# Kernel optimization log

Measured on AMD Instinct MI355X. Metric: run time of the kernel, lower is better.

Reference implementation:

```python
import jax, jax.numpy as jnp
import numpy as np

D_MODEL = 1024
N_HEADS = 16
D_K = 64

def setup_inputs() -> dict:
    key = jax.random.key(0)
    k0, k1, k2, k3, k4 = jax.random.split(key, 5)
    B, S = 4, 4096
    std = 0.02
    x = jax.random.normal(k0, (B, S, D_MODEL), dtype=jnp.float32)
    # nn.Linear weights are [out, in]; init normal(0, 0.02) as in _init_weights
    W_q = std * jax.random.normal(k1, (N_HEADS * D_K, D_MODEL), dtype=jnp.float32)
    W_k = std * jax.random.normal(k2, (N_HEADS * D_K, D_MODEL), dtype=jnp.float32)
    W_v = std * jax.random.normal(k3, (N_HEADS * D_K, D_MODEL), dtype=jnp.float32)
    W_o = std * jax.random.normal(k4, (D_MODEL, N_HEADS * D_K), dtype=jnp.float32)
    return {"x": x, "W_q": W_q, "W_k": W_k, "W_v": W_v, "W_o": W_o}

def reference(x, W_q, W_k, W_v, W_o):
    B, S, _ = x.shape
    H, Dk = N_HEADS, D_K
    # projections (nn.Linear: x @ W.T), reshape to [B, S, H, Dk]
    q = (x @ W_q.T).reshape(B, S, H, Dk)
    k = (x @ W_k.T).reshape(B, S, H, Dk)
    v = (x @ W_v.T).reshape(B, S, H, Dk)
    scale = 1.0 / jnp.sqrt(jnp.float32(Dk))
    # No softmax between the two matmuls -> reassociate (QK^T)V = Q(K^TV),
    # identical math, O(S*d^2) instead of O(S^2*d).
    kv = jnp.einsum('bshd,bshe->bhde', k, v)          # [B, H, Dk, Dk]
    attn = jnp.einsum('bshd,bhde->bshe', q, kv) * scale  # [B, S, H, Dk]
    out = attn.reshape(B, S, H * Dk) @ W_o.T
    return out
```

## Files before the change

### kernel.cpp

```cpp
#include <hip/hip_runtime.h>
#include <hip/hip_bf16.h>
#include <cstdint>


typedef __bf16 bf16x8 __attribute__((ext_vector_type(8)));
typedef float f32x4 __attribute__((ext_vector_type(4)));
typedef unsigned short ushort_t;

__device__ inline void gld_lds16(const void* g, void* l) {
    __builtin_amdgcn_global_load_lds(
        (const __attribute__((address_space(1))) unsigned int*)g,
        (__attribute__((address_space(3))) unsigned int*)l,
        16, 0, 0);
}

__device__ inline ushort_t f2bf(float f) {
    uint32_t u = __float_as_uint(f);
    uint32_t r = (u + 0x7fffu + ((u >> 16) & 1u)) >> 16;
    return (ushort_t)r;
}
__device__ inline float bf2f(ushort_t u) {
    return __uint_as_float((uint32_t)u << 16);
}

__global__ __launch_bounds__(256)
void prep(const float* __restrict__ x, const float* __restrict__ Wk,
          const float* __restrict__ Wv, const float* __restrict__ Wq,
          ushort_t* __restrict__ xb, ushort_t* __restrict__ xbT,
          ushort_t* __restrict__ wkv, ushort_t* __restrict__ wqT)
{
    __shared__ ushort_t lt[64 * 66];
    const int id = blockIdx.x;
    const int t  = threadIdx.x;

    if (id < 4096) {
        const int s0 = (id & 255) * 64;
        const int i0 = (id >> 8) * 64;
#pragma unroll
        for (int c = 0; c < 4; ++c) {
            const int idx = c * 256 + t;
            const int r = idx >> 4, c4 = (idx & 15) * 4;
            const float4 f = *(const float4*)&x[(size_t)(s0 + r) * 1024 + i0 + c4];
            ushort4 o;
            o.x = f2bf(f.x); o.y = f2bf(f.y); o.z = f2bf(f.z); o.w = f2bf(f.w);
            *(ushort4*)&xb[(size_t)(s0 + r) * 1024 + i0 + c4] = o;
            *(uint32_t*)&lt[r * 66 + c4]     = (uint32_t)o.x | ((uint32_t)o.y << 16);
            *(uint32_t*)&lt[r * 66 + c4 + 2] = (uint32_t)o.z | ((uint32_t)o.w << 16);
        }
        __syncthreads();
#pragma unroll
        for (int c = 0; c < 4; ++c) {
            const int idx = c * 256 + t;
            const int ri = idx >> 4, s4 = (idx & 15) * 4;
            ushort4 o;
            o.x = lt[(s4 + 0) * 66 + ri];
            o.y = lt[(s4 + 1) * 66 + ri];
            o.z = lt[(s4 + 2) * 66 + ri];
            o.w = lt[(s4 + 3) * 66 + ri];
            *(ushort4*)&xbT[(size_t)(i0 + ri) * 16384 + s0 + s4] = o;
        }
        return;
    }

    if (id < 5120) {
        const int q  = id - 4096;
        const int qq = (q < 512) ? q : q - 512;
        const float* src = (q < 512) ? Wk : Wv;
        const float* s = src + (size_t)qq * 2048 + t * 8;
        ushort_t* d = wkv + (size_t)q * 2048 + t * 8;
        const float4 f0 = *(const float4*)(s);
        const float4 f1 = *(const float4*)(s + 4);
        ushort4 o0, o1;
        o0.x = f2bf(f0.x); o0.y = f2bf(f0.y); o0.z = f2bf(f0.z); o0.w = f2bf(f0.w);
        o1.x = f2bf(f1.x); o1.y = f2bf(f1.y); o1.z = f2bf(f1.z); o1.w = f2bf(f1.w);
        *(ushort4*)(d)     = o0;
        *(ushort4*)(d + 4) = o1;
        return;
    }

    const int id2 = id - 5120;
    const int r0 = (id2 >> 4) * 64;
    const int c0 = (id2 & 15) * 64;
#pragma unroll
    for (int c = 0; c < 4; ++c) {
        const int idx = c * 256 + t;
        const int r = idx >> 4, c4 = (idx & 15) * 4;
        const float4 f = *(const float4*)&Wq[(size_t)(r0 + r) * 1024 + c0 + c4];
        ushort4 o;
        o.x = f2bf(f.x); o.y = f2bf(f.y); o.z = f2bf(f.z); o.w = f2bf(f.w);
        *(uint32_t*)&lt[r * 66 + c4]     = (uint32_t)o.x | ((uint32_t)o.y << 16);
        *(uint32_t*)&lt[r * 66 + c4 + 2] = (uint32_t)o.z | ((uint32_t)o.w << 16);
    }
    __syncthreads();
#pragma unroll
    for (int c = 0; c < 4; ++c) {
        const int idx = c * 256 + t;
        const int ri = idx >> 4, s4 = (idx & 15) * 4;
        ushort4 o;
        o.x = lt[(s4 + 0) * 66 + ri];
        o.y = lt[(s4 + 1) * 66 + ri];
        o.z = lt[(s4 + 2) * 66 + ri];
        o.w = lt[(s4 + 3) * 66 + ri];
        *(ushort4*)&wqT[(size_t)(c0 + ri) * 1024 + r0 + s4] = o;
    }
}

template <typename OutT>
__global__ __launch_bounds__(256, 4)
void gemm_bt_n64(const ushort_t* __restrict__ A, int lda, long strideA,
                 const ushort_t* __restrict__ B, int ldb, long strideB,
                 OutT* __restrict__ C0, int ldc0, long strideC0, int K)
{
    __shared__ ushort_t lA[128 * 32];
    __shared__ ushort_t lB[64 * 32];

    const int t    = threadIdx.x;
    const int lane = t & 63;
    const int wid  = t >> 6;
    const int z    = blockIdx.z;

    A += (size_t)z * strideA;
    B += (size_t)z * strideB;

    const int m0 = blockIdx.x * 128;
    const int n0 = blockIdx.y * 64;

    const int wm = (wid >> 1) * 64;
    const int wn = (wid & 1) * 32;
    const int mr = lane & 15;
    const int q4 = lane >> 4;

    const int row_a = t >> 2;
    const int seg   = ((t & 3) ^ ((t >> 3) & 3)) * 8;
    const int csw   = (q4 ^ ((mr >> 1) & 3)) * 16;

    f32x4 acc[4][2] = {};

    for (int k0 = 0; k0 < K; k0 += 32) {
        __syncthreads();
        gld_lds16(A + (size_t)(m0 + row_a) * lda + k0 + seg,      (char*)lA + wid * 1024);
        gld_lds16(A + (size_t)(m0 + 64 + row_a) * lda + k0 + seg, (char*)lA + 4096 + wid * 1024);
        gld_lds16(B + (size_t)(n0 + row_a) * ldb + k0 + seg,      (char*)lB + wid * 1024);
        __syncthreads();

        bf16x8 af[4], bf[2];
#pragma unroll
        for (int i = 0; i < 4; ++i)
            af[i] = *(const bf16x8*)((const char*)lA + (wm + i * 16 + mr) * 64 + csw);
#pragma unroll
        for (int j = 0; j < 2; ++j)
            bf[j] = *(const bf16x8*)((const char*)lB + (wn + j * 16 + mr) * 64 + csw);
#pragma unroll
        for (int i = 0; i < 4; ++i)
#pragma unroll
            for (int j = 0; j < 2; ++j)
                acc[i][j] = __builtin_amdgcn_mfma_f32_16x16x32_bf16(af[i], bf[j], acc[i][j], 0, 0, 0);
    }

    OutT* Cw = C0 + (size_t)z * strideC0;
#pragma unroll
    for (int i = 0; i < 4; ++i) {
        const int rbase = m0 + wm + i * 16 + q4 * 4;
#pragma unroll
        for (int j = 0; j < 2; ++j) {
            const int col = n0 + wn + j * 16 + mr;
#pragma unroll
            for (int r = 0; r < 4; ++r) {
                const float v = acc[i][j][r];
                const size_t off = (size_t)(rbase + r) * ldc0 + col;
                if constexpr (sizeof(OutT) == 2) Cw[off] = f2bf(v);
                else                             Cw[off] = v;
            }
        }
    }
}

__global__ __launch_bounds__(256, 2)
void gemm_fin(const ushort_t* __restrict__ A, int lda, long strideA,
              const ushort_t* __restrict__ B, int ldb, long strideB,
              float* __restrict__ C, int ldc, long strideC, int K)
{
    __shared__ char lds[73728];

    const int t    = threadIdx.x;
    const int lane = t & 63;
    const int wid  = t >> 6;

    const int L  = blockIdx.x + (blockIdx.y << 4) + (blockIdx.z << 7);
    const int w  = ((L & 7) << 6) + (L >> 3);
    const int bx = w & 15, by = (w >> 4) & 7, z = w >> 7;

    A += (size_t)z * strideA;
    B += (size_t)z * strideB;

    const int m0 = bx * 256;
    const int n0 = by * 128;

    const int wr = wid >> 1;
    const int wn = wid & 1;
    const int mr = lane & 15;
    const int q4 = lane >> 4;

    const int NT = K >> 5;

    const int row_a = t >> 2;
    const int seg   = ((t & 3) ^ ((t >> 3) & 3)) * 8;
    const int csw   = (q4 ^ ((mr >> 1) & 3)) * 16;

    auto stage = [&](int tgt, int bsel) {
        if (tgt >= NT) return;
        char* base = lds + bsel * 24576 + wid * 1024;
        const ushort_t* gA = A + (size_t)(m0 + row_a) * lda + tgt * 32 + seg;
        gld_lds16(gA,                          base);
        gld_lds16(gA + ((size_t)lda << 6),     base + 4096);
        gld_lds16(gA + ((size_t)lda << 7),     base + 8192);
        gld_lds16(gA + (size_t)lda * 192,      base + 12288);
        const ushort_t* gB = B + (size_t)(n0 + row_a) * ldb + tgt * 32 + seg;
        gld_lds16(gB,                          base + 16384);
        gld_lds16(gB + ((size_t)ldb << 6),     base + 20480);
    };

    bf16x8 af[8], bf[4];
    f32x4 acc[8][4] = {};

    stage(0, 0);
    stage(1, 1);
    asm volatile("s_waitcnt vmcnt(6)" ::: "memory");
    __builtin_amdgcn_s_barrier();

    int cur = 0;
    for (int kt = 0; kt < NT; ++kt) {
        const char* buf = lds + cur * 24576;
#pragma unroll
        for (int i = 0; i < 8; ++i)
            af[i] = *(const bf16x8*)(buf + (wr * 128 + i * 16 + mr) * 64 + csw);
#pragma unroll
        for (int j = 0; j < 4; ++j)
            bf[j] = *(const bf16x8*)(buf + 16384 + (wn * 64 + j * 16 + mr) * 64 + csw);

        int b2 = cur + 2; if (b2 >= 3) b2 -= 3;
        stage(kt + 2, b2);

        asm volatile("s_waitcnt lgkmcnt(0)" ::: "memory");
        __builtin_amdgcn_sched_barrier(0);
        __builtin_amdgcn_s_setprio(1);
#pragma unroll
        for (int i = 0; i < 8; ++i)
#pragma unroll
            for (int j = 0; j < 4; ++j)
                acc[i][j] = __builtin_amdgcn_mfma_f32_16x16x32_bf16(
                    af[i], bf[j], acc[i][j], 0, 0, 0);
        __builtin_amdgcn_s_setprio(0);
        __builtin_amdgcn_sched_barrier(0);

        if (kt + 2 < NT)       asm volatile("s_waitcnt vmcnt(6)" ::: "memory");
        else if (kt + 2 == NT) asm volatile("s_waitcnt vmcnt(0)" ::: "memory");
        __builtin_amdgcn_s_barrier();
        if (++cur == 3) cur = 0;
    }

    float* Cw = C + (size_t)z * strideC;
#pragma unroll
    for (int i = 0; i < 8; ++i) {
        const int rbase = m0 + wr * 128 + i * 16 + q4 * 4;
#pragma unroll
        for (int j = 0; j < 4; ++j) {
            const int col = n0 + wn * 64 + j * 16 + mr;
#pragma unroll
            for (int r = 0; r < 4; ++r)
                Cw[(size_t)(rbase + r) * ldc + col] = acc[i][j][r];
        }
    }
}

__global__ __launch_bounds__(256, 2)
void gemm_gram(const ushort_t* __restrict__ X, ushort_t* __restrict__ Gp)
{
    __shared__ ushort_t lA[128 * 32];
    __shared__ ushort_t lB[128 * 32];

    const int t    = threadIdx.x;
    const int lane = t & 63;
    const int wid  = t >> 6;

    const int z  = blockIdx.x;
    const int bb = z >> 2, ks = z & 3;

    int ti = 0, rem = blockIdx.y;
    while (rem >= 8 - ti) { rem -= 8 - ti; ++ti; }
    const int tj = ti + rem;
    const int m0 = ti * 128;
    const int n0 = tj * 128;

    const ushort_t* A = X + (size_t)bb * 4096 + (size_t)ks * 1024;

    const int wm = (wid >> 1) * 64;
    const int wn = (wid & 1) * 64;
    const int mr = lane & 15;
    const int q4 = lane >> 4;

    const int row_a = t >> 2;
    const int seg   = ((t & 3) ^ ((t >> 3) & 3)) * 8;
    const int csw   = (q4 ^ ((mr >> 1) & 3)) * 16;

    f32x4 acc[4][4] = {};

    for (int k0 = 0; k0 < 1024; k0 += 32) {
        __syncthreads();
        gld_lds16(A + (size_t)(m0 + row_a) * 16384 + k0 + seg,      (char*)lA + wid * 1024);
        gld_lds16(A + (size_t)(m0 + 64 + row_a) * 16384 + k0 + seg, (char*)lA + 4096 + wid * 1024);
        gld_lds16(A + (size_t)(n0 + row_a) * 16384 + k0 + seg,      (char*)lB + wid * 1024);
        gld_lds16(A + (size_t)(n0 + 64 + row_a) * 16384 + k0 + seg, (char*)lB + 4096 + wid * 1024);
        __syncthreads();

        bf16x8 af[4], bf[4];
#pragma unroll
        for (int i = 0; i < 4; ++i)
            af[i] = *(const bf16x8*)((const char*)lA + (wm + i * 16 + mr) * 64 + csw);
#pragma unroll
        for (int j = 0; j < 4; ++j)
            bf[j] = *(const bf16x8*)((const char*)lB + (wn + j * 16 + mr) * 64 + csw);
#pragma unroll
        for (int i = 0; i < 4; ++i)
#pragma unroll
            for (int j = 0; j < 4; ++j)
                acc[i][j] = __builtin_amdgcn_mfma_f32_16x16x32_bf16(af[i], bf[j], acc[i][j], 0, 0, 0);
    }

    ushort_t* Cw = Gp + ((size_t)z << 20);
#pragma unroll
    for (int i = 0; i < 4; ++i) {
        const int rbase = m0 + wm + i * 16 + q4 * 4;
#pragma unroll
        for (int j = 0; j < 4; ++j) {
            const int col = n0 + wn + j * 16 + mr;
#pragma unroll
            for (int r = 0; r < 4; ++r)
                Cw[(size_t)(rbase + r) * 1024 + col] = f2bf(acc[i][j][r]);
        }
    }
}

__global__ __launch_bounds__(256)
void reduce_g_t(const ushort_t* __restrict__ Gp, ushort_t* __restrict__ G)
{
    __shared__ float acc[64 * 65];

    const int t  = threadIdx.x;
    const int b  = blockIdx.y;
    const int tr = blockIdx.x >> 4, tc = blockIdx.x & 15;
    const int sr = (tr <= tc) ? tr : tc;
    const int sc = (tr <= tc) ? tc : tr;
    const bool flip = tr > tc;

#pragma unroll
    for (int p = 0; p < 4; ++p) {
        const int idx = p * 256 + t;
        const int r = idx >> 4, c = (idx & 15) * 4;
        float a0 = 0.f, a1 = 0.f, a2 = 0.f, a3 = 0.f;
#pragma unroll
        for (int ksl = 0; ksl < 4; ++ksl) {
            const ushort4 u = *(const ushort4*)&Gp[((size_t)(b * 4 + ksl) << 20)
                                                   + (size_t)(sr * 64 + r) * 1024 + sc * 64 + c];
            a0 += bf2f(u.x); a1 += bf2f(u.y); a2 += bf2f(u.z); a3 += bf2f(u.w);
        }
        acc[r * 65 + c + 0] = a0;
        acc[r * 65 + c + 1] = a1;
        acc[r * 65 + c + 2] = a2;
        acc[r * 65 + c + 3] = a3;
    }
    __syncthreads();

#pragma unroll
    for (int p = 0; p < 4; ++p) {
        const int idx = p * 256 + t;
        const int r = idx >> 4, c = (idx & 15) * 4;
        float v0, v1, v2, v3;
        if (flip) {
            v0 = acc[(c + 0) * 65 + r];
            v1 = acc[(c + 1) * 65 + r];
            v2 = acc[(c + 2) * 65 + r];
            v3 = acc[(c + 3) * 65 + r];
        } else {
            v0 = acc[r * 65 + c + 0];
            v1 = acc[r * 65 + c + 1];
            v2 = acc[r * 65 + c + 2];
            v3 = acc[r * 65 + c + 3];
        }
        ushort4 o;
        o.x = f2bf(v0); o.y = f2bf(v1); o.z = f2bf(v2); o.w = f2bf(v3);
        *(ushort4*)&G[((size_t)b << 20) + (size_t)(tr * 64 + r) * 1024 + tc * 64 + c] = o;
    }
}

__global__ __launch_bounds__(256)
void kvblk(const ushort_t* __restrict__ H, const ushort_t* __restrict__ Wv,
           float* __restrict__ KVp)
{
    __shared__ ushort_t sH[64 * 132];
    __shared__ ushort_t sV[64 * 132];

    const int t  = threadIdx.x;
    const int is = blockIdx.x;
    const int bh = blockIdx.y;
    const int b  = bh >> 4, h = bh & 15;

    const ushort_t* Hp = H + ((size_t)b << 20) + (size_t)(h * 64) * 1024 + is * 128;
    const ushort_t* Vp = Wv + (size_t)(h * 64) * 1024 + is * 128;

#pragma unroll
    for (int i2 = 0; i2 < 8; ++i2) {
        const int ci = i2 * 256 + t;
        const int r = ci >> 5, c = (ci & 31) * 4;
        *(uint2*)&sH[r * 132 + c] = *(const uint2*)&Hp[(size_t)r * 1024 + c];
        *(uint2*)&sV[r * 132 + c] = *(const uint2*)&Vp[(size_t)r * 1024 + c];
    }
    __syncthreads();

    const int d0 = (t >> 4) * 4;
    const int e0 = (t & 15) * 4;
    float acc[4][4] = {};

#pragma unroll 2
    for (int i4 = 0; i4 < 128; i4 += 4) {
        uint2 hu[4], vu[4];
#pragma unroll
        for (int j = 0; j < 4; ++j) {
            hu[j] = *(const uint2*)&sH[(d0 + j) * 132 + i4];
            vu[j] = *(const uint2*)&sV[(e0 + j) * 132 + i4];
        }
        float hf[4][4], vf[4][4];
#pragma unroll
        for (int j = 0; j < 4; ++j) {
            hf[j][0] = __uint_as_float(hu[j].x << 16);
            hf[j][1] = __uint_as_float(hu[j].x & 0xffff0000u);
            hf[j][2] = __uint_as_float(hu[j].y << 16);
            hf[j][3] = __uint_as_float(hu[j].y & 0xffff0000u);
            vf[j][0] = __uint_as_float(vu[j].x << 16);
            vf[j][1] = __uint_as_float(vu[j].x & 0xffff0000u);
            vf[j][2] = __uint_as_float(vu[j].y << 16);
            vf[j][3] = __uint_as_float(vu[j].y & 0xffff0000u);
        }
#pragma unroll
        for (int ii = 0; ii < 4; ++ii)
#pragma unroll
            for (int di = 0; di < 4; ++di)
#pragma unroll
                for (int ej = 0; ej < 4; ++ej)
                    acc[di][ej] += hf[di][ii] * vf[ej][ii];
    }

    float* outp = KVp + ((size_t)(is * 64 + bh)) * 4096;
#pragma unroll
    for (int i = 0; i < 4; ++i) {
        float4 o; o.x = acc[i][0]; o.y = acc[i][1]; o.z = acc[i][2]; o.w = acc[i][3];
        *(float4*)&outp[(d0 + i) * 64 + e0] = o;
    }
}

__global__ __launch_bounds__(256)
void make_E8(const float* __restrict__ KVp, const float* __restrict__ Wo,
             ushort_t* __restrict__ Et)
{
    __shared__ float skv[64 * 65];
    __shared__ float swo[64 * 65];

    const int t  = threadIdx.x;
    const int bh = blockIdx.y;
    const int b  = bh >> 4, h = bh & 15;
    const int j0 = blockIdx.x * 64;

#pragma unroll
    for (int i = 0; i < 4; ++i) {
        const int idx = t + i * 256;
        const int r = idx >> 4, c = (idx & 15) * 4;
        float4 f; f.x = 0.f; f.y = 0.f; f.z = 0.f; f.w = 0.f;
#pragma unroll
        for (int is = 0; is < 8; ++is) {
            const float4 p = *(const float4*)&KVp[((size_t)(is * 64 + bh)) * 4096
                                                  + r * 64 + c];
            f.x += p.x; f.y += p.y; f.z += p.z; f.w += p.w;
        }
        skv[r * 65 + c + 0] = f.x;
        skv[r * 65 + c + 1] = f.y;
        skv[r * 65 + c + 2] = f.z;
        skv[r * 65 + c + 3] = f.w;
        const float4 g = *(const float4*)&Wo[(size_t)(j0 + r) * 1024 + h * 64 + c];
        swo[r * 65 + c + 0] = g.x;
        swo[r * 65 + c + 1] = g.y;
        swo[r * 65 + c + 2] = g.z;
        swo[r * 65 + c + 3] = g.w;
    }
    __syncthreads();

    const int d0 = (t & 15) * 4;
#pragma unroll
    for (int pass = 0; pass < 4; ++pass) {
        const int jloc = (t >> 4) + pass * 16;
        float s0 = 0.f, s1 = 0.f, s2 = 0.f, s3 = 0.f;
        const float* wrow = &swo[jloc * 65];
#pragma unroll 8
        for (int e = 0; e < 64; ++e) {
            const float w = wrow[e];
            s0 += skv[(d0 + 0) * 65 + e] * w;
            s1 += skv[(d0 + 1) * 65 + e] * w;
            s2 += skv[(d0 + 2) * 65 + e] * w;
            s3 += skv[(d0 + 3) * 65 + e] * w;
        }
        ushort4 o;
        o.x = f2bf(s0 * 0.125f);
        o.y = f2bf(s1 * 0.125f);
        o.z = f2bf(s2 * 0.125f);
        o.w = f2bf(s3 * 0.125f);
        *(ushort4*)&Et[((size_t)b * 1024 + j0 + jloc) * 1024 + h * 64 + d0] = o;
    }
}


extern "C" void kernel_launch(void* const* d_in, const int* in_sizes, int n_in,
                              void* d_out, int out_size, void* d_ws, size_t ws_size,
                              hipStream_t stream)
{
    const float* x  = (const float*)d_in[0];
    const float* Wq = (const float*)d_in[1];
    const float* Wk = (const float*)d_in[2];
    const float* Wv = (const float*)d_in[3];
    const float* Wo = (const float*)d_in[4];
    float* out = (float*)d_out;

    const int B = 4, S = 4096, D = 1024;
    const long MB1 = 1048576;

    char* ws = (char*)d_ws;
    size_t off = 0;
    auto alloc = [&](size_t bytes) -> void* {
        void* p = ws + off;
        off += (bytes + 255) & ~(size_t)255;
        return p;
    };
    ushort_t* xb   = (ushort_t*)alloc((size_t)B * S * D * 2);
    ushort_t* xbT  = (ushort_t*)alloc((size_t)D * B * S * 2);
    ushort_t* wkv  = (ushort_t*)alloc((size_t)2 * D * D * 2);
    ushort_t* wqT  = (ushort_t*)alloc((size_t)D * D * 2);
    ushort_t* Gb   = (ushort_t*)alloc((size_t)B * D * D * 2);
    float*    kvp  = (float*)alloc((size_t)8 * 64 * 4096 * 4);
    ushort_t* Fb   = (ushort_t*)alloc((size_t)B * D * D * 2);
    char*     R1   = (char*)alloc((size_t)16 * MB1 * 2);
    ushort_t* Gp = (ushort_t*)R1;
    ushort_t* Hb = (ushort_t*)R1;
    ushort_t* Et = (ushort_t*)(R1 + 8 * MB1 * 2);
    ushort_t* wkb = wkv;
    ushort_t* wvb = wkv + MB1;

    prep<<<dim3(5376), dim3(256), 0, stream>>>(x, Wk, Wv, Wq, xb, xbT, wkv, wqT);

    gemm_gram<<<dim3(16, 36), dim3(256), 0, stream>>>(xbT, Gp);
    reduce_g_t<<<dim3(256, 4), dim3(256), 0, stream>>>(Gp, Gb);

    gemm_bt_n64<ushort_t><<<dim3(8, 16, 4), dim3(256), 0, stream>>>(
        wkb, D, 0, Gb, D, MB1, Hb, D, MB1, D);

    kvblk<<<dim3(8, 64), dim3(256), 0, stream>>>(Hb, wvb, kvp);

    make_E8<<<dim3(16, 64), dim3(256), 0, stream>>>(kvp, Wo, Et);

    gemm_bt_n64<ushort_t><<<dim3(8, 16, 4), dim3(256), 0, stream>>>(
        Et, D, MB1, wqT, D, 0, Fb, D, (long)D * D, D);

    gemm_fin<<<dim3(16, 8, 4), dim3(256), 0, stream>>>(
        xb, D, (long)S * D, Fb, D, (long)D * D, out, D, (long)S * D, D);
}
```

Baseline: 308.3 us.

## Triple-buffer gram GEMM loads and widen prep blocks for more loads in flight

The gram GEMM moves from a single LDS buffer with two barriers per k-step to a three-stage global→LDS pipeline. Loads for tile k+2 are issued while the current tile is computed, using explicit vmcnt waits, a single barrier per step and raised wave priority around the MFMAs. The prep kernel now has each block handle twice (x) or four times (Wk/Wv) as much data, issuing all loads before converting, so fewer blocks run with more memory-level parallelism. LDS use grows to 48KB per gram block, which may limit occupancy, and the hand-written waitcnt logic is fragile.

```diff
diff --git a/kernel.cpp b/kernel.cpp
--- a/kernel.cpp
+++ b/kernel.cpp
@@ -29,67 +29,92 @@
           ushort_t* __restrict__ xb, ushort_t* __restrict__ xbT,
           ushort_t* __restrict__ wkv, ushort_t* __restrict__ wqT)
 {
-    __shared__ ushort_t lt[64 * 66];
+    __shared__ ushort_t lt[2][64 * 66];
     const int id = blockIdx.x;
     const int t  = threadIdx.x;
 
-    if (id < 4096) {
+    if (id < 2048) {
         const int s0 = (id & 255) * 64;
-        const int i0 = (id >> 8) * 64;
-#pragma unroll
-        for (int c = 0; c < 4; ++c) {
+        const int i0 = (id >> 8) * 128;
+
+        float4 f[8];
+#pragma unroll
+        for (int c = 0; c < 8; ++c) {
             const int idx = c * 256 + t;
-            const int r = idx >> 4, c4 = (idx & 15) * 4;
-            const float4 f = *(const float4*)&x[(size_t)(s0 + r) * 1024 + i0 + c4];
+            const int r  = idx >> 5;
+            const int c4 = (idx & 31) * 4;
+            f[c] = *(const float4*)&x[(size_t)(s0 + r) * 1024 + i0 + c4];
+        }
+#pragma unroll
+        for (int c = 0; c < 8; ++c) {
+            const int idx = c * 256 + t;
+            const int r  = idx >> 5;
+            const int c4 = (idx & 31) * 4;
             ushort4 o;
-            o.x = f2bf(f.x); o.y = f2bf(f.y); o.z = f2bf(f.z); o.w = f2bf(f.w);
+            o.x = f2bf(f[c].x); o.y = f2bf(f[c].y);
+            o.z = f2bf(f[c].z); o.w = f2bf(f[c].w);
             *(ushort4*)&xb[(size_t)(s0 + r) * 1024 + i0 + c4] = o;
-            *(uint32_t*)&lt[r * 66 + c4]     = (uint32_t)o.x | ((uint32_t)o.y << 16);
-            *(uint32_t*)&lt[r * 66 + c4 + 2] = (uint32_t)o.z | ((uint32_t)o.w << 16);
+            const int half = c4 >> 6;
+            const int cc   = c4 & 63;
+            *(uint32_t*)&lt[half][r * 66 + cc]     = (uint32_t)o.x | ((uint32_t)o.y << 16);
+            *(uint32_t*)&lt[half][r * 66 + cc + 2] = (uint32_t)o.z | ((uint32_t)o.w << 16);
         }
         __syncthreads();
 #pragma unroll
-        for (int c = 0; c < 4; ++c) {
-            const int idx = c * 256 + t;
-            const int ri = idx >> 4, s4 = (idx & 15) * 4;
+        for (int c = 0; c < 8; ++c) {
+            const int idx  = c * 256 + t;
+            const int rig  = idx >> 4;
+            const int s4   = (idx & 15) * 4;
+            const int half = rig >> 6;
+            const int ri   = rig & 63;
             ushort4 o;
-            o.x = lt[(s4 + 0) * 66 + ri];
-            o.y = lt[(s4 + 1) * 66 + ri];
-            o.z = lt[(s4 + 2) * 66 + ri];
-            o.w = lt[(s4 + 3) * 66 + ri];
-            *(ushort4*)&xbT[(size_t)(i0 + ri) * 16384 + s0 + s4] = o;
+            o.x = lt[half][(s4 + 0) * 66 + ri];
+            o.y = lt[half][(s4 + 1) * 66 + ri];
+            o.z = lt[half][(s4 + 2) * 66 + ri];
+            o.w = lt[half][(s4 + 3) * 66 + ri];
+            *(ushort4*)&xbT[(size_t)(i0 + rig) * 16384 + s0 + s4] = o;
         }
         return;
     }
 
-    if (id < 5120) {
-        const int q  = id - 4096;
-        const int qq = (q < 512) ? q : q - 512;
-        const float* src = (q < 512) ? Wk : Wv;
-        const float* s = src + (size_t)qq * 2048 + t * 8;
-        ushort_t* d = wkv + (size_t)q * 2048 + t * 8;
-        const float4 f0 = *(const float4*)(s);
-        const float4 f1 = *(const float4*)(s + 4);
-        ushort4 o0, o1;
-        o0.x = f2bf(f0.x); o0.y = f2bf(f0.y); o0.z = f2bf(f0.z); o0.w = f2bf(f0.w);
-        o1.x = f2bf(f1.x); o1.y = f2bf(f1.y); o1.z = f2bf(f1.z); o1.w = f2bf(f1.w);
-        *(ushort4*)(d)     = o0;
-        *(ushort4*)(d + 4) = o1;
+    if (id < 2304) {
+        const int q  = id - 2048;
+        const int qq = (q < 128) ? q : q - 128;
+        const float* src = (q < 128) ? Wk : Wv;
+        float4 f[8];
+#pragma unroll
+        for (int c = 0; c < 8; ++c)
+            f[c] = *(const float4*)&src[(size_t)qq * 8192 + c * 1024 + t * 4];
+        ushort_t* d = wkv + (size_t)q * 8192;
+#pragma unroll
+        for (int c = 0; c < 8; ++c) {
+            ushort4 o;
+            o.x = f2bf(f[c].x); o.y = f2bf(f[c].y);
+            o.z = f2bf(f[c].z); o.w = f2bf(f[c].w);
+            *(ushort4*)&d[c * 1024 + t * 4] = o;
+        }
         return;
     }
 
-    const int id2 = id - 5120;
+    const int id2 = id - 2304;
     const int r0 = (id2 >> 4) * 64;
     const int c0 = (id2 & 15) * 64;
+    float4 f[4];
 #pragma unroll
     for (int c = 0; c < 4; ++c) {
         const int idx = c * 256 + t;
         const int r = idx >> 4, c4 = (idx & 15) * 4;
-        const float4 f = *(const float4*)&Wq[(size_t)(r0 + r) * 1024 + c0 + c4];
+        f[c] = *(const float4*)&Wq[(size_t)(r0 + r) * 1024 + c0 + c4];
+    }
+#pragma unroll
+    for (int c = 0; c < 4; ++c) {
+        const int idx = c * 256 + t;
+        const int r = idx >> 4, c4 = (idx & 15) * 4;
         ushort4 o;
-        o.x = f2bf(f.x); o.y = f2bf(f.y); o.z = f2bf(f.z); o.w = f2bf(f.w);
-        *(uint32_t*)&lt[r * 66 + c4]     = (uint32_t)o.x | ((uint32_t)o.y << 16);
-        *(uint32_t*)&lt[r * 66 + c4 + 2] = (uint32_t)o.z | ((uint32_t)o.w << 16);
+        o.x = f2bf(f[c].x); o.y = f2bf(f[c].y);
+        o.z = f2bf(f[c].z); o.w = f2bf(f[c].w);
+        *(uint32_t*)&lt[0][r * 66 + c4]     = (uint32_t)o.x | ((uint32_t)o.y << 16);
+        *(uint32_t*)&lt[0][r * 66 + c4 + 2] = (uint32_t)o.z | ((uint32_t)o.w << 16);
     }
     __syncthreads();
 #pragma unroll
@@ -97,10 +122,10 @@
         const int idx = c * 256 + t;
         const int ri = idx >> 4, s4 = (idx & 15) * 4;
         ushort4 o;
-        o.x = lt[(s4 + 0) * 66 + ri];
-        o.y = lt[(s4 + 1) * 66 + ri];
-        o.z = lt[(s4 + 2) * 66 + ri];
-        o.w = lt[(s4 + 3) * 66 + ri];
+        o.x = lt[0][(s4 + 0) * 66 + ri];
+        o.y = lt[0][(s4 + 1) * 66 + ri];
+        o.z = lt[0][(s4 + 2) * 66 + ri];
+        o.w = lt[0][(s4 + 3) * 66 + ri];
         *(ushort4*)&wqT[(size_t)(c0 + ri) * 1024 + r0 + s4] = o;
     }
 }
@@ -274,10 +299,9 @@
 }
 
 __global__ __launch_bounds__(256, 2)
-void gemm_gram(const ushort_t* __restrict__ X, ushort_t* __restrict__ Gp)
-{
-    __shared__ ushort_t lA[128 * 32];
-    __shared__ ushort_t lB[128 * 32];
+void gemm_gram3(const ushort_t* __restrict__ X, ushort_t* __restrict__ Gp)
+{
+    __shared__ char lds[49152];
 
     const int t    = threadIdx.x;
     const int lane = t & 63;
@@ -293,6 +317,7 @@
     const int n0 = tj * 128;
 
     const ushort_t* A = X + (size_t)bb * 4096 + (size_t)ks * 1024;
+    const int NT = 32;
 
     const int wm = (wid >> 1) * 64;
     const int wn = (wid & 1) * 64;
@@ -303,28 +328,54 @@
     const int seg   = ((t & 3) ^ ((t >> 3) & 3)) * 8;
     const int csw   = (q4 ^ ((mr >> 1) & 3)) * 16;
 
+    auto stage = [&](int tgt, int bsel) {
+        if (tgt >= NT) return;
+        char* base = lds + bsel * 16384 + wid * 1024;
+        const ushort_t* gA = A + (size_t)(m0 + row_a) * 16384 + tgt * 32 + seg;
+        gld_lds16(gA,                        base);
+        gld_lds16(gA + ((size_t)16384 << 6), base + 4096);
+        const ushort_t* gB = A + (size_t)(n0 + row_a) * 16384 + tgt * 32 + seg;
+        gld_lds16(gB,                        base + 8192);
+        gld_lds16(gB + ((size_t)16384 << 6), base + 12288);
+    };
+
+    bf16x8 af[4], bf[4];
     f32x4 acc[4][4] = {};
 
-    for (int k0 = 0; k0 < 1024; k0 += 32) {
-        __syncthreads();
-        gld_lds16(A + (size_t)(m0 + row_a) * 16384 + k0 + seg,      (char*)lA + wid * 1024);
-        gld_lds16(A + (size_t)(m0 + 64 + row_a) * 16384 + k0 + seg, (char*)lA + 4096 + wid * 1024);
-        gld_lds16(A + (size_t)(n0 + row_a) * 16384 + k0 + seg,      (char*)lB + wid * 1024);
-        gld_lds16(A + (size_t)(n0 + 64 + row_a) * 16384 + k0 + seg, (char*)lB + 4096 + wid * 1024);
-        __syncthreads();
-
-        bf16x8 af[4], bf[4];
+    stage(0, 0);
+    stage(1, 1);
+    asm volatile("s_waitcnt vmcnt(4)" ::: "memory");
+    __builtin_amdgcn_s_barrier();
+
+    int cur = 0;
+    for (int kt = 0; kt < NT; ++kt) {
+        const char* buf = lds + cur * 16384;
 #pragma unroll
         for (int i = 0; i < 4; ++i)
-            af[i] = *(const bf16x8*)((const char*)lA + (wm + i * 16 + mr) * 64 + csw);
+            af[i] = *(const bf16x8*)(buf + (wm + i * 16 + mr) * 64 + csw);
 #pragma unroll
         for (int j = 0; j < 4; ++j)
-            bf[j] = *(const bf16x8*)((const char*)lB + (wn + j * 16 + mr) * 64 + csw);
+            bf[j] = *(const bf16x8*)(buf + 8192 + (wn + j * 16 + mr) * 64 + csw);
+
+        int b2 = cur + 2; if (b2 >= 3) b2 -= 3;
+        stage(kt + 2, b2);
+
+        asm volatile("s_waitcnt lgkmcnt(0)" ::: "memory");
+        __builtin_amdgcn_sched_barrier(0);
+        __builtin_amdgcn_s_setprio(1);
 #pragma unroll
         for (int i = 0; i < 4; ++i)
 #pragma unroll
             for (int j = 0; j < 4; ++j)
-                acc[i][j] = __builtin_amdgcn_mfma_f32_16x16x32_bf16(af[i], bf[j], acc[i][j], 0, 0, 0);
+                acc[i][j] = __builtin_amdgcn_mfma_f32_16x16x32_bf16(
+                    af[i], bf[j], acc[i][j], 0, 0, 0);
+        __builtin_amdgcn_s_setprio(0);
+        __builtin_amdgcn_sched_barrier(0);
+
+        if (kt + 2 < NT)       asm volatile("s_waitcnt vmcnt(4)" ::: "memory");
+        else if (kt + 2 == NT) asm volatile("s_waitcnt vmcnt(0)" ::: "memory");
+        __builtin_amdgcn_s_barrier();
+        if (++cur == 3) cur = 0;
     }
 
     ushort_t* Cw = Gp + ((size_t)z << 20);
@@ -552,9 +603,9 @@
     ushort_t* wkb = wkv;
     ushort_t* wvb = wkv + MB1;
 
-    prep<<<dim3(5376), dim3(256), 0, stream>>>(x, Wk, Wv, Wq, xb, xbT, wkv, wqT);
-
-    gemm_gram<<<dim3(16, 36), dim3(256), 0, stream>>>(xbT, Gp);
+    prep<<<dim3(2560), dim3(256), 0, stream>>>(x, Wk, Wv, Wq, xb, xbT, wkv, wqT);
+
+    gemm_gram3<<<dim3(16, 36), dim3(256), 0, stream>>>(xbT, Gp);
     reduce_g_t<<<dim3(256, 4), dim3(256), 0, stream>>>(Gp, Gb);
 
     gemm_bt_n64<ushort_t><<<dim3(8, 16, 4), dim3(256), 0, stream>>>(
```

New measurement: 310.9 us. No clear change (+0.8%).
